# Kernel tuning notes

Measured on AMD Instinct MI355X. Metric: run time of the kernel, lower is better.

## Reference

```python
import jax, jax.numpy as jnp
import numpy as np

E = 500_000
D = 128
A = 16
HID = 128
G = 25_000
IN = 2 * D + A  # 272


def setup_inputs() -> dict:
    key = jax.random.key(0)
    ks = jax.random.split(key, 8)
    src_emb = jax.random.normal(ks[0], (E, D), dtype=jnp.float32)
    dst_emb = jax.random.normal(ks[1], (E, D), dtype=jnp.float32)
    edge_attr = jax.random.normal(ks[2], (E, A), dtype=jnp.float32)
    group_index = jax.random.randint(ks[3], (E,), 0, G, dtype=jnp.int64)
    # MLP params: LazyLinear(IN->HID), Linear(HID->1)
    W1 = jax.random.normal(ks[4], (IN, HID), dtype=jnp.float32) * (1.0 / np.sqrt(IN))
    b1 = jnp.zeros((HID,), dtype=jnp.float32)
    W2 = jax.random.normal(ks[5], (HID, 1), dtype=jnp.float32) * (1.0 / np.sqrt(HID))
    b2 = jnp.zeros((1,), dtype=jnp.float32)
    return {
        "src_emb": src_emb,
        "dst_emb": dst_emb,
        "edge_attr": edge_attr,
        "W1": W1,
        "b1": b1,
        "W2": W2,
        "b2": b2,
        "group_index": group_index,
        "num_groups": G,
    }


def reference(src_emb, dst_emb, edge_attr, W1, b1, W2, b2, group_index, num_groups):
    # features: [E, 2D+A]
    features = jnp.concatenate([src_emb, dst_emb, edge_attr], axis=-1)
    h = jax.nn.relu(features @ W1 + b1)            # [E, HID]
    logits = (h @ W2 + b2)[:, 0]                   # [E]
    # single-pass segment softmax (replaces per-group python loop)
    lf = logits.astype(jnp.float32)
    seg_max = jax.ops.segment_max(lf, group_index, num_segments=num_groups)  # [G]
    # empty segments give -inf max; edges never index them, so safe
    ex = jnp.exp(lf - seg_max[group_index])        # [E]
    seg_sum = jax.ops.segment_sum(ex, group_index, num_segments=num_groups)  # [G]
    weights = (ex / seg_sum[group_index]).astype(logits.dtype)[:, None]      # [E, 1]
    return weights, logits
```

## Files before the change

### kernel.cpp

```cpp
#include <hip/hip_runtime.h>
#include <stdint.h>

#define E_N   500000
#define G_N   25000
#define HIDN  128
#define KIN   272
#define NKSTEP 9
#define WB_ELEMS 36864

typedef short bfrag_t __attribute__((ext_vector_type(8)));
typedef float accf4  __attribute__((ext_vector_type(4)));

__device__ __forceinline__ uint32_t pack2_bf16(float a, float b) {
    uint32_t ua = __builtin_bit_cast(uint32_t, a) + 0x8000u;
    uint32_t ub = __builtin_bit_cast(uint32_t, b) + 0x8000u;
    return __builtin_amdgcn_perm(ub, ua, 0x07060302u);
}

__global__ void prep_kernel(const float* __restrict__ W1, float* __restrict__ seg_sum,
                            ushort* __restrict__ Wb) {
    int t = blockIdx.x * 256 + threadIdx.x;
    if (t < G_N) seg_sum[t] = 0.0f;
    int j    = t & 7;
    int lane = (t >> 3) & 63;
    int sb   = t >> 9;
    int b    = sb & 7;
    int s    = sb >> 3;
    int k    = s * 32 + (lane >> 4) * 8 + j;
    int n    = b * 16 + (lane & 15);
    ushort v = 0;
    if (k < KIN) {
        uint32_t u = __builtin_bit_cast(uint32_t, W1[k * HIDN + n]);
        u += 0x7FFFu + ((u >> 16) & 1u);
        v = (ushort)(u >> 16);
    }
    Wb[t] = v;
}

__launch_bounds__(512, 4)
__global__ void mlp_kernel(const float* __restrict__ src, const float* __restrict__ dst,
                           const float* __restrict__ attr, const ushort* __restrict__ Wb,
                           const float* __restrict__ b1, const float* __restrict__ W2,
                           const float* __restrict__ b2, const int* __restrict__ gidx,
                           float* __restrict__ logits_out, float* __restrict__ ex_out,
                           float* __restrict__ seg_sum) {
    __shared__ __align__(16) ushort Blds[WB_ELEMS];

    const int tid  = threadIdx.x;
    const int lane = tid & 63;
    const int wave = tid >> 6;
    const int m    = lane & 15;
    const int q    = lane >> 4;
    const int rowbase = blockIdx.x * 256 + wave * 32;

    #pragma unroll
    for (int i = 0; i < 9; ++i) {
        int c = i * 512 + tid;
        ((uint4*)Blds)[c] = ((const uint4*)Wb)[c];
    }
    __syncthreads();

    const int  r0 = rowbase + m,  r1 = rowbase + 16 + m;
    const bool v0 = r0 < E_N,     v1 = r1 < E_N;

    accf4 acc[2][8];
    #pragma unroll
    for (int a = 0; a < 2; ++a)
        #pragma unroll
        for (int b = 0; b < 8; ++b)
            acc[a][b] = (accf4)(0.0f);

    #pragma unroll
    for (int s = 0; s < NKSTEP; ++s) {
        bfrag_t af[2];
        #pragma unroll
        for (int a = 0; a < 2; ++a) {
            const int  rr = a ? r1 : r0;
            const bool vv = a ? v1 : v0;
            float4 x0 = {0.f, 0.f, 0.f, 0.f}, x1 = {0.f, 0.f, 0.f, 0.f};
            if (s < 8) {
                const float* base  = (s < 4) ? src : dst;
                const int coloff   = (s < 4) ? s * 32 : (s - 4) * 32;
                const float* p = base + (size_t)rr * 128 + coloff + q * 8;
                if (vv) { x0 = ((const float4*)p)[0]; x1 = ((const float4*)p)[1]; }
            } else {
                if (vv && q < 2) {
                    const float* p = attr + (size_t)rr * 16 + q * 8;
                    x0 = ((const float4*)p)[0]; x1 = ((const float4*)p)[1];
                }
            }
            uint4 u;
            u.x = pack2_bf16(x0.x, x0.y);
            u.y = pack2_bf16(x0.z, x0.w);
            u.z = pack2_bf16(x1.x, x1.y);
            u.w = pack2_bf16(x1.z, x1.w);
            af[a] = *(bfrag_t*)&u;
        }

        #pragma unroll
        for (int b = 0; b < 8; ++b) {
            bfrag_t bf = *(const bfrag_t*)&Blds[(size_t)((s * 8 + b) * 64 + lane) * 8];
            #pragma unroll
            for (int a = 0; a < 2; ++a)
                acc[a][b] = __builtin_amdgcn_mfma_f32_16x16x32_bf16(af[a], bf, acc[a][b], 0, 0, 0);
        }
    }

    float w2v[8], b1v[8];
    #pragma unroll
    for (int b = 0; b < 8; ++b) {
        w2v[b] = W2[b * 16 + m];
        b1v[b] = b1[b * 16 + m];
    }
    const float bias2 = b2[0];

    #pragma unroll
    for (int a = 0; a < 2; ++a) {
        float p4[4] = {0.f, 0.f, 0.f, 0.f};
        #pragma unroll
        for (int b = 0; b < 8; ++b)
            #pragma unroll
            for (int rr = 0; rr < 4; ++rr) {
                float h = acc[a][b][rr] + b1v[b];
                h = h > 0.f ? h : 0.f;
                p4[rr] += h * w2v[b];
            }
        #pragma unroll
        for (int rr = 0; rr < 4; ++rr) {
            float v = p4[rr];
            v += __shfl_xor(v, 1);
            v += __shfl_xor(v, 2);
            v += __shfl_xor(v, 4);
            v += __shfl_xor(v, 8);
            if (m == 0) {
                int grow = rowbase + a * 16 + q * 4 + rr;
                if (grow < E_N) {
                    float logit = v + bias2;
                    logits_out[grow] = logit;
                    float ex = __expf(logit);
                    ex_out[grow] = ex;
                    atomicAdd(&seg_sum[gidx[grow]], ex);
                }
            }
        }
    }
}

__global__ void norm_kernel(const float* __restrict__ ex, const float* __restrict__ seg_sum,
                            const int* __restrict__ gidx, float* __restrict__ wout) {
    int e = blockIdx.x * 256 + threadIdx.x;
    if (e < E_N) wout[e] = ex[e] / seg_sum[gidx[e]];
}

extern "C" void kernel_launch(void* const* d_in, const int* in_sizes, int n_in,
                              void* d_out, int out_size, void* d_ws, size_t ws_size,
                              hipStream_t stream) {
    const float* src  = (const float*)d_in[0];
    const float* dst  = (const float*)d_in[1];
    const float* attr = (const float*)d_in[2];
    const float* W1   = (const float*)d_in[3];
    const float* b1   = (const float*)d_in[4];
    const float* W2   = (const float*)d_in[5];
    const float* b2   = (const float*)d_in[6];
    const int*   gidx = (const int*)d_in[7];

    float* weights_out = (float*)d_out;
    float* logits_out  = (float*)d_out + E_N;

    char* ws = (char*)d_ws;
    ushort* Wb  = (ushort*)ws;
    float*  seg = (float*)(ws + 73728);
    float*  ex  = (float*)(ws + 173728);

    prep_kernel<<<144, 256, 0, stream>>>(W1, seg, Wb);

    const int nblk = (E_N + 255) / 256;
    mlp_kernel<<<nblk, 512, 0, stream>>>(src, dst, attr, Wb, b1, W2, b2, gidx,
                                         logits_out, ex, seg);
    norm_kernel<<<(E_N + 255) / 256, 256, 0, stream>>>(ex, seg, gidx, weights_out);
}
```

Measured before the change: 537.8 us.

## Double-buffer activation tiles in LDS via async global-to-LDS loads

Replaces direct per-lane global loads of the src/dst/attr rows with async global_load_lds copies into a double-buffered, XOR-swizzled LDS tile, prefetching the next K-step while the current one runs MFMAs. The weight tile is also loaded with global_load_lds. The aim is to hide HBM latency and keep the matrix units fed. In exchange, LDS use rises to about 136KB per block, occupancy hints drop from 4 to 2, and two barriers per K-step are added. The attr step reads with (gba & 63) and clamped rows rather than zero-masking, relying on the zero-padded weights for K beyond 272.

```diff
diff --git a/kernel.cpp b/kernel.cpp
--- a/kernel.cpp
+++ b/kernel.cpp
@@ -7,6 +7,8 @@
 #define KIN   272
 #define NKSTEP 9
 #define WB_ELEMS 36864
+#define ROWS   256
+#define ABUF_F 8192
 
 typedef short bfrag_t __attribute__((ext_vector_type(8)));
 typedef float accf4  __attribute__((ext_vector_type(4)));
@@ -15,6 +17,12 @@
     uint32_t ua = __builtin_bit_cast(uint32_t, a) + 0x8000u;
     uint32_t ub = __builtin_bit_cast(uint32_t, b) + 0x8000u;
     return __builtin_amdgcn_perm(ub, ua, 0x07060302u);
+}
+
+__device__ __forceinline__ void gl2lds16(const void* g, void* l) {
+    __builtin_amdgcn_global_load_lds(
+        (const __attribute__((address_space(1))) void*)g,
+        (__attribute__((address_space(3))) void*)l, 16, 0, 0);
 }
 
 __global__ void prep_kernel(const float* __restrict__ W1, float* __restrict__ seg_sum,
@@ -37,13 +45,14 @@
     Wb[t] = v;
 }
 
-__launch_bounds__(512, 4)
+__launch_bounds__(512, 2)
 __global__ void mlp_kernel(const float* __restrict__ src, const float* __restrict__ dst,
                            const float* __restrict__ attr, const ushort* __restrict__ Wb,
                            const float* __restrict__ b1, const float* __restrict__ W2,
                            const float* __restrict__ b2, const int* __restrict__ gidx,
                            float* __restrict__ logits_out, float* __restrict__ ex_out,
                            float* __restrict__ seg_sum) {
+    __shared__ __align__(16) float  Alds[2][ABUF_F];
     __shared__ __align__(16) ushort Blds[WB_ELEMS];
 
     const int tid  = threadIdx.x;
@@ -51,17 +60,29 @@
     const int wave = tid >> 6;
     const int m    = lane & 15;
     const int q    = lane >> 4;
-    const int rowbase = blockIdx.x * 256 + wave * 32;
+    const int rowbase = blockIdx.x * ROWS;
 
     #pragma unroll
     for (int i = 0; i < 9; ++i) {
-        int c = i * 512 + tid;
-        ((uint4*)Blds)[c] = ((const uint4*)Wb)[c];
-    }
-    __syncthreads();
-
-    const int  r0 = rowbase + m,  r1 = rowbase + 16 + m;
-    const bool v0 = r0 < E_N,     v1 = r1 < E_N;
+        const int c = i * 512 + tid;
+        gl2lds16((const char*)Wb + (size_t)c * 16, (char*)Blds + c * 16);
+    }
+
+    int rowi[4], gba[4], loff[4];
+    #pragma unroll
+    for (int i = 0; i < 4; ++i) {
+        const int c  = i * 512 + tid;
+        const int rl = c >> 3;
+        gba[i] = ((c & 7) * 16) ^ ((rl & 7) << 4);
+        const int row = rowbase + rl;
+        rowi[i] = row < E_N ? row : (E_N - 1);
+        loff[i] = c * 16;
+    }
+
+    #pragma unroll
+    for (int i = 0; i < 4; ++i)
+        gl2lds16((const char*)src + (size_t)rowi[i] * 512 + gba[i],
+                 (char*)Alds[0] + loff[i]);
 
     accf4 acc[2][8];
     #pragma unroll
@@ -70,40 +91,65 @@
         for (int b = 0; b < 8; ++b)
             acc[a][b] = (accf4)(0.0f);
 
-    #pragma unroll
+    const int rl0 = wave * 32 + m;
+    const int rl1 = rl0 + 16;
+    const int swz = (rl0 & 7) << 4;
+    const int cb0 = (q * 32) ^ swz;
+    const int cb1 = (q * 32 + 16) ^ swz;
+
     for (int s = 0; s < NKSTEP; ++s) {
+        if (s + 1 < NKSTEP) {
+            const int sn = s + 1;
+            char* abuf = (char*)Alds[sn & 1];
+            if (sn < 8) {
+                const char* bse = (const char*)(sn < 4 ? src : dst);
+                const int co = (sn & 3) * 128;
+                #pragma unroll
+                for (int i = 0; i < 4; ++i)
+                    gl2lds16(bse + (size_t)rowi[i] * 512 + co + gba[i], abuf + loff[i]);
+            } else {
+                #pragma unroll
+                for (int i = 0; i < 4; ++i)
+                    gl2lds16((const char*)attr + (size_t)rowi[i] * 64 + (gba[i] & 63),
+                             abuf + loff[i]);
+            }
+            asm volatile("s_waitcnt vmcnt(4)" ::: "memory");
+        } else {
+            asm volatile("s_waitcnt vmcnt(0)" ::: "memory");
+        }
+        __builtin_amdgcn_s_barrier();
+
+        const char* rp0 = (const char*)Alds[s & 1] + rl0 * 128;
+        const char* rp1 = (const char*)Alds[s & 1] + rl1 * 128;
         bfrag_t af[2];
-        #pragma unroll
-        for (int a = 0; a < 2; ++a) {
-            const int  rr = a ? r1 : r0;
-            const bool vv = a ? v1 : v0;
-            float4 x0 = {0.f, 0.f, 0.f, 0.f}, x1 = {0.f, 0.f, 0.f, 0.f};
-            if (s < 8) {
-                const float* base  = (s < 4) ? src : dst;
-                const int coloff   = (s < 4) ? s * 32 : (s - 4) * 32;
-                const float* p = base + (size_t)rr * 128 + coloff + q * 8;
-                if (vv) { x0 = ((const float4*)p)[0]; x1 = ((const float4*)p)[1]; }
-            } else {
-                if (vv && q < 2) {
-                    const float* p = attr + (size_t)rr * 16 + q * 8;
-                    x0 = ((const float4*)p)[0]; x1 = ((const float4*)p)[1];
-                }
-            }
+        {
+            float4 x0 = *(const float4*)(rp0 + cb0);
+            float4 x1 = *(const float4*)(rp0 + cb1);
             uint4 u;
             u.x = pack2_bf16(x0.x, x0.y);
             u.y = pack2_bf16(x0.z, x0.w);
             u.z = pack2_bf16(x1.x, x1.y);
             u.w = pack2_bf16(x1.z, x1.w);
-            af[a] = *(bfrag_t*)&u;
+            af[0] = *(bfrag_t*)&u;
+        }
+        {
+            float4 x0 = *(const float4*)(rp1 + cb0);
+            float4 x1 = *(const float4*)(rp1 + cb1);
+            uint4 u;
+            u.x = pack2_bf16(x0.x, x0.y);
+            u.y = pack2_bf16(x0.z, x0.w);
+            u.z = pack2_bf16(x1.x, x1.y);
+            u.w = pack2_bf16(x1.z, x1.w);
+            af[1] = *(bfrag_t*)&u;
         }
 
         #pragma unroll
         for (int b = 0; b < 8; ++b) {
             bfrag_t bf = *(const bfrag_t*)&Blds[(size_t)((s * 8 + b) * 64 + lane) * 8];
-            #pragma unroll
-            for (int a = 0; a < 2; ++a)
-                acc[a][b] = __builtin_amdgcn_mfma_f32_16x16x32_bf16(af[a], bf, acc[a][b], 0, 0, 0);
-        }
+            acc[0][b] = __builtin_amdgcn_mfma_f32_16x16x32_bf16(af[0], bf, acc[0][b], 0, 0, 0);
+            acc[1][b] = __builtin_amdgcn_mfma_f32_16x16x32_bf16(af[1], bf, acc[1][b], 0, 0, 0);
+        }
+        __builtin_amdgcn_s_barrier();
     }
 
     float w2v[8], b1v[8];
@@ -113,6 +159,7 @@
         b1v[b] = b1[b * 16 + m];
     }
     const float bias2 = b2[0];
+    const int wrow = rowbase + wave * 32;
 
     #pragma unroll
     for (int a = 0; a < 2; ++a) {
@@ -133,7 +180,7 @@
             v += __shfl_xor(v, 4);
             v += __shfl_xor(v, 8);
             if (m == 0) {
-                int grow = rowbase + a * 16 + q * 4 + rr;
+                int grow = wrow + a * 16 + q * 4 + rr;
                 if (grow < E_N) {
                     float logit = v + bias2;
                     logits_out[grow] = logit;
@@ -174,7 +221,7 @@
 
     prep_kernel<<<144, 256, 0, stream>>>(W1, seg, Wb);
 
-    const int nblk = (E_N + 255) / 256;
+    const int nblk = (E_N + ROWS - 1) / ROWS;
     mlp_kernel<<<nblk, 512, 0, stream>>>(src, dst, attr, Wb, b1, W2, b2, gidx,
                                          logits_out, ex, seg);
     norm_kernel<<<(E_N + 255) / 256, 256, 0, stream>>>(ex, seg, gidx, weights_out);
```

After: 543.2 us. No clear change (+1.0%).
